# Kernel tuning notes

Hardware: AMD Instinct MI355X
Metric: run time of the kernel (lower is better)

The kernel has to match this reference:

```python
import jax, jax.numpy as jnp
import numpy as np
from jax import lax

# dims: B=2, C=dim=64, H=W=128 -> N=16384 tokens; d_inner=128, d_state=16, dt_rank=4, d_conv=4

def setup_inputs() -> dict:
    key = jax.random.key(0)
    ks = jax.random.split(key, 8)
    def n(k, shp, scale=0.02):
        return jax.random.normal(k, shp, jnp.float32) * scale
    d_inner, d_state, dt_rank = 128, 16, 4
    return {
        "x": jax.random.normal(ks[0], (2, 64, 128, 128), jnp.float32),
        "ln_w": jnp.ones((64,), jnp.float32),
        "ln_b": jnp.zeros((64,), jnp.float32),
        "in_proj_w": n(ks[1], (2 * d_inner, 64)),
        "conv_w": n(ks[2], (d_inner, 1, 4), 0.1),
        "conv_b": jnp.zeros((d_inner,), jnp.float32),
        "x_proj_w": n(ks[3], (dt_rank + 2 * d_state, d_inner)),
        "dt_proj_w": n(ks[4], (d_inner, dt_rank), 0.5),
        "dt_proj_b": n(ks[5], (d_inner,), 0.1),
        "A_log": jnp.log(jnp.broadcast_to(jnp.arange(1, d_state + 1, dtype=jnp.float32), (d_inner, d_state))),
        "D_param": jnp.ones((d_inner,), jnp.float32),
        "out_proj_w": n(ks[6], (64, d_inner)),
        "out_proj_b": jnp.zeros((64,), jnp.float32),
    }


def reference(x, ln_w, ln_b, in_proj_w, conv_w, conv_b, x_proj_w,
              dt_proj_w, dt_proj_b, A_log, D_param, out_proj_w, out_proj_b):
    B, C, H, W = x.shape
    d_inner = in_proj_w.shape[0] // 2
    d_state = A_log.shape[1]
    dt_rank = dt_proj_w.shape[1]
    eps = 1e-5

    # feature2token + channel LayerNorm (Restormer WithBias LN over C)
    t = x.reshape(B, C, H * W).transpose(0, 2, 1)  # [B, N, C]
    mu = jnp.mean(t, axis=-1, keepdims=True)
    var = jnp.var(t, axis=-1, keepdims=True)
    t = (t - mu) * lax.rsqrt(var + eps) * ln_w + ln_b

    # in_proj -> x, z
    xz = jnp.einsum('bnc,dc->bnd', t, in_proj_w)  # [B, N, 2*d_inner]
    x_in, z = jnp.split(xz, 2, axis=-1)

    # depthwise causal conv1d (k=4, pad left 3), then SiLU
    u = lax.conv_general_dilated(
        x_in.transpose(0, 2, 1), conv_w,
        window_strides=(1,), padding=[(3, 0)],
        feature_group_count=d_inner,
        dimension_numbers=('NCH', 'OIH', 'NCH'))
    u = jax.nn.silu(u + conv_b[None, :, None]).transpose(0, 2, 1)  # [B, N, d_inner]

    # x_proj -> dt, B, C of the SSM
    x_dbl = jnp.einsum('bnd,ed->bne', u, x_proj_w)
    dt_r = x_dbl[..., :dt_rank]
    Bmat = x_dbl[..., dt_rank:dt_rank + d_state]   # [B, N, d_state]
    Cmat = x_dbl[..., dt_rank + d_state:]          # [B, N, d_state]
    dt = jax.nn.softplus(jnp.einsum('bnr,dr->bnd', dt_r, dt_proj_w) + dt_proj_b)

    # selective scan: h_t = exp(dt*A) h_{t-1} + dt*B*u
    A = -jnp.exp(A_log)  # [d_inner, d_state]
    deltaA = jnp.exp(jnp.einsum('bnd,ds->bnds', dt, A))
    deltaBu = jnp.einsum('bnd,bns,bnd->bnds', dt, Bmat, u)

    def combine(c1, c2):
        a1, b1 = c1
        a2, b2 = c2
        return a2 * a1, a2 * b1 + b2

    _, h = lax.associative_scan(combine, (deltaA, deltaBu), axis=1)  # h: [B, N, d_inner, d_state]

    y = jnp.einsum('bnds,bns->bnd', h, Cmat) + u * D_param
    y = y * jax.nn.silu(z)
    out = jnp.einsum('bnd,cd->bnc', y, out_proj_w) + out_proj_b  # [B, N, C]

    # token2feature
    return out.transpose(0, 2, 1).reshape(B, C, H, W)
```

## Files before the change

kernel.cpp:

```cpp
#include <hip/hip_runtime.h>
#include <math.h>

#define NTOK 16384
#define DIN  128
#define NCH  512
#define CHL  32
#define NG   32
#define GCH  16

__device__ __forceinline__ float silu_f(float x)    { return x / (1.f + __expf(-x)); }
__device__ __forceinline__ float softplus_f(float x){ return (x > 20.f) ? x : log1pf(__expf(x)); }

__global__ __launch_bounds__(256) void k1_ln_inproj(
    const float* __restrict__ x, const float* __restrict__ lnw,
    const float* __restrict__ lnb, const float* __restrict__ Win,
    float* __restrict__ xin, float* __restrict__ zbuf)
{
  __shared__ __align__(16) float bufA[64*68];
  __shared__ __align__(16) float bufB[64*68];
  __shared__ float ps[256], pq[256], mu[64], rs[64];

  int t = threadIdx.x;
  int b  = blockIdx.x >> 8;
  int n0 = (blockIdx.x & 255) << 6;
  const float* xb = x + ((size_t)b*64)*NTOK;

  int tok = t & 63, quad = t >> 6;
  float s0 = 0.f, s1 = 0.f;
  for (int i = 0; i < 16; ++i) {
    int c = i*4 + quad;
    float v = xb[(size_t)c*NTOK + n0 + tok];
    bufA[c*68 + tok] = v;
    s0 += v; s1 += v*v;
  }
  ps[t] = s0; pq[t] = s1;
  __syncthreads();
  if (t < 64) {
    float m = ps[t] + ps[64+t] + ps[128+t] + ps[192+t];
    float q = pq[t] + pq[64+t] + pq[128+t] + pq[192+t];
    m *= 0.015625f;
    q = q*0.015625f - m*m;
    mu[t] = m; rs[t] = rsqrtf(q + 1e-5f);
  }
  __syncthreads();

  {
    int c = t & 63, tq = t >> 6;
    float wv = lnw[c], bv = lnb[c];
    #pragma unroll
    for (int i = 0; i < 4; ++i) {
      int tok4 = tq*4 + i;
      float4 f = *(const float4*)&bufA[c*68 + tok4*4];
      float vals[4] = {f.x, f.y, f.z, f.w};
      #pragma unroll
      for (int k = 0; k < 4; ++k) {
        int tk = tok4*4 + k;
        bufB[tk*68 + c] = (vals[k] - mu[tk]) * rs[tk] * wv + bv;
      }
    }
  }

  int tokg = t & 15, dg = t >> 4;
  const float4* TB = (const float4*)bufB;
  for (int q = 0; q < 4; ++q) {
    __syncthreads();
    for (int i = 0; i < 16; ++i) {
      int idx = i*256 + t;
      int c = idx & 63, dd = idx >> 6;
      bufA[dd*68 + c] = Win[(q*64 + dd)*64 + c];
    }
    __syncthreads();
    const float4* WA = (const float4*)bufA;
    float acc[4][4];
    #pragma unroll
    for (int i = 0; i < 4; ++i)
      #pragma unroll
      for (int j = 0; j < 4; ++j) acc[i][j] = 0.f;
    #pragma unroll 4
    for (int c4 = 0; c4 < 16; ++c4) {
      float4 tv[4], wv[4];
      #pragma unroll
      for (int i = 0; i < 4; ++i) tv[i] = TB[(tokg + 16*i)*17 + c4];
      #pragma unroll
      for (int j = 0; j < 4; ++j) wv[j] = WA[(dg + 16*j)*17 + c4];
      #pragma unroll
      for (int i = 0; i < 4; ++i)
        #pragma unroll
        for (int j = 0; j < 4; ++j)
          acc[i][j] += tv[i].x*wv[j].x + tv[i].y*wv[j].y
                     + tv[i].z*wv[j].z + tv[i].w*wv[j].w;
    }
    #pragma unroll
    for (int i = 0; i < 4; ++i) {
      long n = (long)b*NTOK + n0 + tokg + 16*i;
      #pragma unroll
      for (int j = 0; j < 4; ++j) {
        int dd = dg + 16*j;
        if (q < 2) xin[n*128 + q*64 + dd] = acc[i][j];
        else       zbuf[n*128 + (q-2)*64 + dd] = silu_f(acc[i][j]);
      }
    }
  }
}

__global__ __launch_bounds__(256) void k2_conv(
    const float* __restrict__ xin, const float* __restrict__ cw,
    const float* __restrict__ cb, float* __restrict__ u)
{
  int t = threadIdx.x;
  int d = t & 127;
  long g0 = (long)blockIdx.x*16 + (t >> 7)*8;
  int n = (int)(g0 & (NTOK-1));
  float w0 = cw[d*4], w1 = cw[d*4+1], w2 = cw[d*4+2], w3 = cw[d*4+3];
  float cbv = cb[d];
  float xa = (n >= 3) ? xin[(g0-3)*128 + d] : 0.f;
  float xb = (n >= 2) ? xin[(g0-2)*128 + d] : 0.f;
  float xc = (n >= 1) ? xin[(g0-1)*128 + d] : 0.f;
  #pragma unroll
  for (int j = 0; j < 8; ++j) {
    float xd = xin[(g0+j)*128 + d];
    u[(g0+j)*128 + d] = silu_f(w0*xa + w1*xb + w2*xc + w3*xd + cbv);
    xa = xb; xb = xc; xc = xd;
  }
}

__global__ __launch_bounds__(256) void k3_xproj_dt(
    const float* __restrict__ u, const float* __restrict__ Wx,
    const float* __restrict__ Wdt, const float* __restrict__ db,
    float* __restrict__ dt, float* __restrict__ Bm, float* __restrict__ Cm)
{
  __shared__ __align__(16) float wx[36*128];
  __shared__ float wdtT[4*128];
  __shared__ __align__(16) float xdbl[64*40];
  int t = threadIdx.x;
  for (int i = t; i < 1152; i += 256)
    *(float4*)&wx[i*4] = *(const float4*)&Wx[i*4];
  for (int i = t; i < 512; i += 256)
    wdtT[(i&3)*128 + (i>>2)] = Wdt[i];
  __syncthreads();

  long tok0 = (long)blockIdx.x * 64;
  int tok = t & 63, grp = t >> 6;
  const float* urow = u + (tok0 + tok)*128;

  float acc[9];
  #pragma unroll
  for (int e = 0; e < 9; ++e) acc[e] = 0.f;
  #pragma unroll 8
  for (int d4 = 0; d4 < 32; ++d4) {
    float4 uv = *(const float4*)&urow[d4*4];
    #pragma unroll
    for (int e = 0; e < 9; ++e) {
      float4 wv = *(const float4*)&wx[(grp*9+e)*128 + d4*4];
      acc[e] += uv.x*wv.x + uv.y*wv.y + uv.z*wv.z + uv.w*wv.w;
    }
  }
  #pragma unroll
  for (int e = 0; e < 9; ++e) xdbl[tok*40 + grp*9 + e] = acc[e];
  __syncthreads();

  {
    int tk = t >> 2, q = t & 3;
    float4 bv = *(const float4*)&xdbl[tk*40 + 4  + q*4];
    float4 cv = *(const float4*)&xdbl[tk*40 + 20 + q*4];
    *(float4*)&Bm[(tok0+tk)*16 + q*4] = bv;
    *(float4*)&Cm[(tok0+tk)*16 + q*4] = cv;
  }
  int d = t & 127, th = t >> 7;
  float w0 = wdtT[d], w1 = wdtT[128+d], w2 = wdtT[256+d], w3 = wdtT[384+d];
  float bias = db[d];
  for (int j = 0; j < 32; ++j) {
    int tk = th*32 + j;
    float a = bias + xdbl[tk*40]*w0 + xdbl[tk*40+1]*w1
                   + xdbl[tk*40+2]*w2 + xdbl[tk*40+3]*w3;
    dt[(tok0+tk)*128 + d] = softplus_f(a);
  }
}

__global__ __launch_bounds__(256) void k4a_local(
    const float* __restrict__ dt, const float* __restrict__ u,
    const float* __restrict__ Bm, const float* __restrict__ Alog,
    float* __restrict__ carP, float* __restrict__ carH)
{
  int t = threadIdx.x;
  int d = t >> 1, sh = t & 1;
  int b = blockIdx.x / NCH, ch = blockIdx.x % NCH;
  long nb = (long)b*NTOK + (long)ch*CHL;
  float A[8], h[8], P[8];
  #pragma unroll
  for (int k = 0; k < 2; ++k) {
    float4 a = *(const float4*)&Alog[d*16 + sh*8 + k*4];
    A[k*4+0] = -__expf(a.x); A[k*4+1] = -__expf(a.y);
    A[k*4+2] = -__expf(a.z); A[k*4+3] = -__expf(a.w);
  }
  #pragma unroll
  for (int s = 0; s < 8; ++s) { h[s] = 0.f; P[s] = 1.f; }
  for (int i = 0; i < CHL; ++i) {
    long n = nb + i;
    float dtv = dt[n*128 + d];
    float uv  = u [n*128 + d];
    float du  = dtv * uv;
    float Bv[8];
    #pragma unroll
    for (int k = 0; k < 2; ++k) {
      float4 v = *(const float4*)&Bm[n*16 + sh*8 + k*4];
      Bv[k*4]=v.x; Bv[k*4+1]=v.y; Bv[k*4+2]=v.z; Bv[k*4+3]=v.w;
    }
    #pragma unroll
    for (int s = 0; s < 8; ++s) {
      float dA = __expf(dtv * A[s]);
      h[s] = dA*h[s] + du*Bv[s];
      P[s] *= dA;
    }
  }
  long cbs = ((long)(b*NCH + ch)*128 + d)*16 + sh*8;
  #pragma unroll
  for (int k = 0; k < 2; ++k) {
    *(float4*)&carP[cbs + k*4] = make_float4(P[k*4],P[k*4+1],P[k*4+2],P[k*4+3]);
    *(float4*)&carH[cbs + k*4] = make_float4(h[k*4],h[k*4+1],h[k*4+2],h[k*4+3]);
  }
}

__global__ __launch_bounds__(256) void k4b1_group(
    float* __restrict__ cP, float* __restrict__ cH,
    float* __restrict__ Pg, float* __restrict__ Hg)
{
  int idx = blockIdx.x*256 + threadIdx.x;
  int rem = idx & 2047;
  int g   = (idx >> 11) & (NG-1);
  int b   = idx >> 16;
  float P = 1.f, H = 0.f;
  long base = ((long)b*NCH + g*GCH)*2048 + rem;
  #pragma unroll 4
  for (int j = 0; j < GCH; ++j) {
    long a = base + (long)j*2048;
    float p = cP[a], h = cH[a];
    cP[a] = P; cH[a] = H;
    H = p*H + h;
    P = p*P;
  }
  long ga = ((long)b*NG + g)*2048 + rem;
  Pg[ga] = P; Hg[ga] = H;
}

__global__ __launch_bounds__(256) void k4b2_carry(
    const float* __restrict__ Pg, float* __restrict__ Hg)
{
  int idx = blockIdx.x*256 + threadIdx.x;
  int b = idx >> 11, rem = idx & 2047;
  float H = 0.f;
  #pragma unroll 4
  for (int g = 0; g < NG; ++g) {
    long a = ((long)b*NG + g)*2048 + rem;
    float p = Pg[a], h = Hg[a];
    Hg[a] = H;
    H = p*H + h;
  }
}

__global__ __launch_bounds__(256) void k4c_apply(
    const float* __restrict__ dt, const float* __restrict__ u,
    const float* __restrict__ Bm, const float* __restrict__ Cm,
    const float* __restrict__ Alog, const float* __restrict__ Dp,
    const float* __restrict__ zs, const float* __restrict__ pPre,
    const float* __restrict__ hPre, const float* __restrict__ Hg,
    float* __restrict__ yz)
{
  int t = threadIdx.x;
  int d = t >> 1, sh = t & 1;
  int b = blockIdx.x / NCH, ch = blockIdx.x % NCH;
  long nb = (long)b*NTOK + (long)ch*CHL;
  float A[8], h[8];
  #pragma unroll
  for (int k = 0; k < 2; ++k) {
    float4 a = *(const float4*)&Alog[d*16 + sh*8 + k*4];
    A[k*4+0] = -__expf(a.x); A[k*4+1] = -__expf(a.y);
    A[k*4+2] = -__expf(a.z); A[k*4+3] = -__expf(a.w);
  }
  long cbs = ((long)(b*NCH + ch)*128 + d)*16 + sh*8;
  long gbs = ((long)b*NG + (ch >> 4))*2048 + d*16 + sh*8;
  #pragma unroll
  for (int k = 0; k < 2; ++k) {
    float4 hp = *(const float4*)&hPre[cbs + k*4];
    float4 pp = *(const float4*)&pPre[cbs + k*4];
    float4 gi = *(const float4*)&Hg[gbs + k*4];
    h[k*4+0] = hp.x + pp.x*gi.x; h[k*4+1] = hp.y + pp.y*gi.y;
    h[k*4+2] = hp.z + pp.z*gi.z; h[k*4+3] = hp.w + pp.w*gi.w;
  }
  float Dv = Dp[d];
  for (int i = 0; i < CHL; ++i) {
    long n = nb + i;
    float dtv = dt[n*128 + d];
    float uv  = u [n*128 + d];
    float du  = dtv * uv;
    float Bv[8], Cv[8];
    #pragma unroll
    for (int k = 0; k < 2; ++k) {
      float4 v = *(const float4*)&Bm[n*16 + sh*8 + k*4];
      Bv[k*4]=v.x; Bv[k*4+1]=v.y; Bv[k*4+2]=v.z; Bv[k*4+3]=v.w;
      float4 w = *(const float4*)&Cm[n*16 + sh*8 + k*4];
      Cv[k*4]=w.x; Cv[k*4+1]=w.y; Cv[k*4+2]=w.z; Cv[k*4+3]=w.w;
    }
    float y = 0.f;
    #pragma unroll
    for (int s = 0; s < 8; ++s) {
      float dA = __expf(dtv * A[s]);
      h[s] = dA*h[s] + du*Bv[s];
      y += h[s]*Cv[s];
    }
    y += __shfl_xor(y, 1);
    if (sh == 0)
      yz[n*128 + d] = (y + uv*Dv) * zs[n*128 + d];
  }
}

__global__ __launch_bounds__(256) void k6_outproj(
    const float* __restrict__ yz, const float* __restrict__ Wout,
    const float* __restrict__ ob, float* __restrict__ out)
{
  __shared__ __align__(16) float wo[64*132];
  __shared__ __align__(16) float yl[32*132];
  int t = threadIdx.x;
  long tok0 = (long)blockIdx.x * 32;
  for (int i = 0; i < 8; ++i) {
    int g = i*256 + t; int c = g >> 5, q = g & 31;
    *(float4*)&wo[c*132 + q*4] = *(const float4*)&Wout[c*128 + q*4];
  }
  for (int i = 0; i < 4; ++i) {
    int g = i*256 + t; int tok = g >> 5, q = g & 31;
    *(float4*)&yl[tok*132 + q*4] = *(const float4*)&yz[(tok0 + tok)*128 + q*4];
  }
  __syncthreads();
  int tp = t & 15;
  int tg = t >> 4;
  float acc[4][2] = {{0.f}};
  for (int d4 = 0; d4 < 32; ++d4) {
    float4 y0 = *(const float4*)&yl[tg*132 + d4*4];
    float4 y1 = *(const float4*)&yl[(tg+16)*132 + d4*4];
    #pragma unroll
    for (int cc = 0; cc < 4; ++cc) {
      float4 wv = *(const float4*)&wo[(tp + 16*cc)*132 + d4*4];
      acc[cc][0] += wv.x*y0.x + wv.y*y0.y + wv.z*y0.z + wv.w*y0.w;
      acc[cc][1] += wv.x*y1.x + wv.y*y1.y + wv.z*y1.z + wv.w*y1.w;
    }
  }
  int b  = (int)(tok0 / NTOK);
  long n0 = tok0 % NTOK;
  #pragma unroll
  for (int cc = 0; cc < 4; ++cc) {
    int c = tp + 16*cc;
    float bias = ob[c];
    out[((long)b*64 + c)*NTOK + n0 + tg     ] = acc[cc][0] + bias;
    out[((long)b*64 + c)*NTOK + n0 + tg + 16] = acc[cc][1] + bias;
  }
}

extern "C" void kernel_launch(void* const* d_in, const int* in_sizes, int n_in,
                              void* d_out, int out_size, void* d_ws, size_t ws_size,
                              hipStream_t stream)
{
  (void)in_sizes; (void)n_in; (void)out_size; (void)ws_size;
  const float* x    = (const float*)d_in[0];
  const float* lnw  = (const float*)d_in[1];
  const float* lnb  = (const float*)d_in[2];
  const float* Win  = (const float*)d_in[3];
  const float* cw   = (const float*)d_in[4];
  const float* cb   = (const float*)d_in[5];
  const float* Wx   = (const float*)d_in[6];
  const float* Wdt  = (const float*)d_in[7];
  const float* db   = (const float*)d_in[8];
  const float* Alog = (const float*)d_in[9];
  const float* Dp   = (const float*)d_in[10];
  const float* Wout = (const float*)d_in[11];
  const float* ob   = (const float*)d_in[12];
  float* out = (float*)d_out;

  float* w   = (float*)d_ws;
  float* xin = w;
  float* z   = w + 4194304;
  float* u   = w + 8388608;
  float* dt  = w + 12582912;
  float* Bm  = w + 16777216;
  float* Cm  = w + 17301504;
  float* cP  = w + 17825792;
  float* cH  = w + 19922944;
  float* Pg  = w + 22020096;
  float* Hg  = w + 22151168;
  float* yz  = w + 22282240;

  k1_ln_inproj<<<512, 256, 0, stream>>>(x, lnw, lnb, Win, xin, z);
  k2_conv     <<<2048,256, 0, stream>>>(xin, cw, cb, u);
  k3_xproj_dt <<<512, 256, 0, stream>>>(u, Wx, Wdt, db, dt, Bm, Cm);
  k4a_local   <<<1024,256, 0, stream>>>(dt, u, Bm, Alog, cP, cH);
  k4b1_group  <<<512, 256, 0, stream>>>(cP, cH, Pg, Hg);
  k4b2_carry  <<<16,  256, 0, stream>>>(Pg, Hg);
  k4c_apply   <<<1024,256, 0, stream>>>(dt, u, Bm, Cm, Alog, Dp, z, cP, cH, Hg, yz);
  k6_outproj  <<<1024,256, 0, stream>>>(yz, Wout, ob, out);
}
```

Measured before the change: 155.7 us.

## Keep in_proj weight rows in registers and stream tokens from LDS

The in_proj GEMM in the LN kernel is restructured. Each thread now holds one full 64-wide weight row in registers and loops over the 64 tokens, reading them from LDS as broadcasts. Previously the weights were staged through shared memory in four chunks with a 4x4 register tile. This removes the repeated weight staging and the syncs around it, and gives coalesced stores along d. The cost is 64 extra VGPRs per thread, which may lower occupancy, and a lower FMA-to-LDS-load ratio.

```diff
diff --git a/kernel.cpp b/kernel.cpp
--- a/kernel.cpp
+++ b/kernel.cpp
@@ -24,6 +24,11 @@
   int b  = blockIdx.x >> 8;
   int n0 = (blockIdx.x & 255) << 6;
   const float* xb = x + ((size_t)b*64)*NTOK;
+
+  float4 wreg[16];
+  #pragma unroll
+  for (int i = 0; i < 16; ++i)
+    wreg[i] = *(const float4*)&Win[t*64 + i*4];
 
   int tok = t & 63, quad = t >> 6;
   float s0 = 0.f, s1 = 0.f;
@@ -59,47 +64,33 @@
       }
     }
   }
-
-  int tokg = t & 15, dg = t >> 4;
-  const float4* TB = (const float4*)bufB;
-  for (int q = 0; q < 4; ++q) {
-    __syncthreads();
-    for (int i = 0; i < 16; ++i) {
-      int idx = i*256 + t;
-      int c = idx & 63, dd = idx >> 6;
-      bufA[dd*68 + c] = Win[(q*64 + dd)*64 + c];
-    }
-    __syncthreads();
-    const float4* WA = (const float4*)bufA;
-    float acc[4][4];
-    #pragma unroll
-    for (int i = 0; i < 4; ++i)
+  __syncthreads();
+
+  bool zhalf = (t >= 128);
+  float* outp = zhalf ? zbuf : xin;
+  int d = t & 127;
+  long nbase = (long)b*NTOK + n0;
+  for (int n = 0; n < 64; n += 2) {
+    const float* r0 = &bufB[n*68];
+    const float* r1 = r0 + 68;
+    float a0[4] = {0.f,0.f,0.f,0.f}, a1[4] = {0.f,0.f,0.f,0.f};
+    #pragma unroll
+    for (int i = 0; i < 4; ++i) {
       #pragma unroll
-      for (int j = 0; j < 4; ++j) acc[i][j] = 0.f;
-    #pragma unroll 4
-    for (int c4 = 0; c4 < 16; ++c4) {
-      float4 tv[4], wv[4];
-      #pragma unroll
-      for (int i = 0; i < 4; ++i) tv[i] = TB[(tokg + 16*i)*17 + c4];
-      #pragma unroll
-      for (int j = 0; j < 4; ++j) wv[j] = WA[(dg + 16*j)*17 + c4];
-      #pragma unroll
-      for (int i = 0; i < 4; ++i)
-        #pragma unroll
-        for (int j = 0; j < 4; ++j)
-          acc[i][j] += tv[i].x*wv[j].x + tv[i].y*wv[j].y
-                     + tv[i].z*wv[j].z + tv[i].w*wv[j].w;
-    }
-    #pragma unroll
-    for (int i = 0; i < 4; ++i) {
-      long n = (long)b*NTOK + n0 + tokg + 16*i;
-      #pragma unroll
-      for (int j = 0; j < 4; ++j) {
-        int dd = dg + 16*j;
-        if (q < 2) xin[n*128 + q*64 + dd] = acc[i][j];
-        else       zbuf[n*128 + (q-2)*64 + dd] = silu_f(acc[i][j]);
+      for (int p = 0; p < 4; ++p) {
+        int c4 = p*4 + i;
+        float4 wv = wreg[c4];
+        float4 t0 = *(const float4*)&r0[c4*4];
+        a0[p] += t0.x*wv.x + t0.y*wv.y + t0.z*wv.z + t0.w*wv.w;
+        float4 t1 = *(const float4*)&r1[c4*4];
+        a1[p] += t1.x*wv.x + t1.y*wv.y + t1.z*wv.z + t1.w*wv.w;
       }
     }
+    float y0 = (a0[0] + a0[1]) + (a0[2] + a0[3]);
+    float y1 = (a1[0] + a1[1]) + (a1[2] + a1[3]);
+    if (zhalf) { y0 = silu_f(y0); y1 = silu_f(y1); }
+    outp[(nbase + n    )*128 + d] = y0;
+    outp[(nbase + n + 1)*128 + d] = y1;
   }
 }
 
```

Measured after the change: 161.3 us. 3.5% more time.
